# Kernel optimization log

Measured on AMD Instinct MI355X. Metric: run time of the kernel, lower is better.

## Reference

```python
import jax, jax.numpy as jnp
import numpy as np

BN_EPS = 1e-5


def conv1x1(x, w, b):
    # x: [B,C,H,W], w: [O,C], b: [O] -> [B,O,H,W]
    return jnp.einsum('bchw,oc->bohw', x, w) + b[None, :, None, None]


def setup_inputs() -> dict:
    key = jax.random.key(0)
    ks = jax.random.split(key, 11)
    B, C, H, W = 8, 1024, 64, 32
    hid = 64  # C * rd_ratio (1/16)
    s = 0.02
    return {
        'x': jax.random.normal(ks[0], (B, C, H, W), dtype=jnp.float32),
        'theta_w': jax.random.normal(ks[1], (hid, C), dtype=jnp.float32) * s,
        'theta_b': jax.random.normal(ks[2], (hid,), dtype=jnp.float32) * s,
        'phi_w': jax.random.normal(ks[3], (hid, C), dtype=jnp.float32) * s,
        'phi_b': jax.random.normal(ks[4], (hid,), dtype=jnp.float32) * s,
        'g_w': jax.random.normal(ks[5], (hid, C), dtype=jnp.float32) * s,
        'g_b': jax.random.normal(ks[6], (hid,), dtype=jnp.float32) * s,
        'w_w': jax.random.normal(ks[7], (C, hid), dtype=jnp.float32) * s,
        'w_b': jax.random.normal(ks[8], (C,), dtype=jnp.float32) * s,
        'bn_gamma': jax.random.normal(ks[9], (C,), dtype=jnp.float32) * 0.1 + 1.0,
        'bn_beta': jax.random.normal(ks[10], (C,), dtype=jnp.float32) * 0.1,
    }


def reference(x, theta_w, theta_b, phi_w, phi_b, g_w, g_b, w_w, w_b, bn_gamma, bn_beta):
    B, C, H, W = x.shape
    hid = theta_w.shape[0]
    N = H * W
    theta = conv1x1(x, theta_w, theta_b).reshape(B, hid, N).transpose(0, 2, 1)  # [B,N,d]
    phi = conv1x1(x, phi_w, phi_b).reshape(B, hid, N)                           # [B,d,N]
    g = conv1x1(x, g_w, g_b).reshape(B, hid, N).transpose(0, 2, 1)              # [B,N,d]
    f = jnp.einsum('bnd,bdm->bnm', theta, phi) / N                              # [B,N,N]
    y = jnp.einsum('bnm,bmd->bnd', f, g)                                        # [B,N,d]
    y = y.transpose(0, 2, 1).reshape(B, hid, H, W)
    wy = conv1x1(y, w_w, w_b)                                                   # [B,C,H,W]
    # BatchNorm2d in training mode: batch statistics over (B,H,W), biased variance
    mean = wy.mean(axis=(0, 2, 3), keepdims=True)
    var = wy.var(axis=(0, 2, 3), keepdims=True)
    norm = (wy - mean) * jax.lax.rsqrt(var + BN_EPS)
    out = norm * bn_gamma[None, :, None, None] + bn_beta[None, :, None, None]
    return out + x
```

## Files before the change

### kernel.cpp

```cpp
#include <hip/hip_runtime.h>

#define B_    8
#define C_    1024
#define HID   64
#define N_    2048
#define RTOT  192

typedef __attribute__((ext_vector_type(8))) short   bf16x8;
typedef __attribute__((ext_vector_type(8))) unsigned short ush8;
typedef __attribute__((ext_vector_type(4))) unsigned short ush4;
typedef __attribute__((ext_vector_type(4))) float   f32x4;

#define WSB_WBF   ((size_t)0)
#define WSB_TPG   ((size_t)393216)
#define WSB_THT   ((size_t)6684672)
#define WSB_M     ((size_t)8781824)
#define WSB_G     ((size_t)8912896)
#define WSB_S     ((size_t)9043968)
#define WSB_WMBF  ((size_t)9046016)
#define WSB_SC    ((size_t)10094592)
#define WSB_SH    ((size_t)10098688)

static __device__ __forceinline__ unsigned short f2bf(float f) {
    union { float f; unsigned u; } v; v.f = f;
    unsigned r = v.u + 0x7fffu + ((v.u >> 16) & 1u);
    return (unsigned short)(r >> 16);
}
static __device__ __forceinline__ float bf2f(unsigned short h) {
    union { unsigned u; float f; } v; v.u = ((unsigned)h) << 16;
    return v.f;
}

__global__ __launch_bounds__(256) void wcvt(
    const float* __restrict__ tw, const float* __restrict__ pw,
    const float* __restrict__ gw, unsigned short* __restrict__ wbf)
{
    int idx = blockIdx.x * 256 + threadIdx.x;
    int r = idx >> 10, k = idx & 1023;
    float v = (r < 64) ? tw[(size_t)r * 1024 + k]
            : (r < 128) ? pw[(size_t)(r - 64) * 1024 + k]
                        : gw[(size_t)(r - 128) * 1024 + k];
    wbf[idx] = f2bf(v);
}

__global__ __launch_bounds__(256, 2) void proj_mfma(
    const float* __restrict__ x, const unsigned short* __restrict__ wbf,
    const float* __restrict__ tb, const float* __restrict__ pb,
    const float* __restrict__ gb, unsigned short* __restrict__ tpgbf,
    unsigned short* __restrict__ thT)
{
    const int b = blockIdx.y, n0 = blockIdx.x * 32;
    const int t = threadIdx.x, w = t >> 6, L = t & 63;
    const int lr = L & 15, q = L >> 4;
    __shared__ unsigned short A_lds[32][520];

    const float* xb = x + (size_t)b * C_ * N_ + n0;
    const unsigned short* bp = wbf + ((size_t)(48 * w + lr)) * 1024 + q * 8;

    f32x4 acc[2][3] = {};

#pragma unroll
    for (int ph = 0; ph < 2; ph++) {
        if (ph) __syncthreads();
#pragma unroll
        for (int i = 0; i < 8; i++) {
            int p = t + 256 * i;
            int n4 = p & 7;
            int c  = ((p >> 3) << 1);
            f32x4 v0 = *(const f32x4*)(xb + (size_t)(512 * ph + c) * N_ + n4 * 4);
            f32x4 v1 = *(const f32x4*)(xb + (size_t)(512 * ph + c + 1) * N_ + n4 * 4);
#pragma unroll
            for (int r = 0; r < 4; r++) {
                unsigned val = (unsigned)f2bf(v0[r]) | ((unsigned)f2bf(v1[r]) << 16);
                *(unsigned*)&A_lds[n4 * 4 + r][c] = val;
            }
        }
        __syncthreads();
#pragma unroll
        for (int ks = 0; ks < 16; ks++) {
            const int kg = ph * 512 + ks * 32;
            bf16x8 B0 = *(const bf16x8*)(bp + kg);
            bf16x8 B1 = *(const bf16x8*)(bp + 16 * 1024 + kg);
            bf16x8 B2 = *(const bf16x8*)(bp + 32 * 1024 + kg);
            bf16x8 A0 = *(const bf16x8*)&A_lds[lr][ks * 32 + q * 8];
            bf16x8 A1 = *(const bf16x8*)&A_lds[16 + lr][ks * 32 + q * 8];
            acc[0][0] = __builtin_amdgcn_mfma_f32_16x16x32_bf16(A0, B0, acc[0][0], 0, 0, 0);
            acc[0][1] = __builtin_amdgcn_mfma_f32_16x16x32_bf16(A0, B1, acc[0][1], 0, 0, 0);
            acc[0][2] = __builtin_amdgcn_mfma_f32_16x16x32_bf16(A0, B2, acc[0][2], 0, 0, 0);
            acc[1][0] = __builtin_amdgcn_mfma_f32_16x16x32_bf16(A1, B0, acc[1][0], 0, 0, 0);
            acc[1][1] = __builtin_amdgcn_mfma_f32_16x16x32_bf16(A1, B1, acc[1][1], 0, 0, 0);
            acc[1][2] = __builtin_amdgcn_mfma_f32_16x16x32_bf16(A1, B2, acc[1][2], 0, 0, 0);
        }
    }

#pragma unroll
    for (int i = 0; i < 2; i++)
#pragma unroll
        for (int j = 0; j < 3; j++) {
            int rcol = 48 * w + 16 * j + lr;
            float bias = (rcol < 64) ? tb[rcol]
                       : (rcol < 128) ? pb[rcol - 64] : gb[rcol - 128];
            ush4 o;
#pragma unroll
            for (int rr = 0; rr < 4; rr++) o[rr] = f2bf(acc[i][j][rr] + bias);
            *(ush4*)(tpgbf + ((size_t)b * RTOT + rcol) * N_ + n0 + 16 * i + q * 4) = o;
            if (rcol < 64) {
#pragma unroll
                for (int rr = 0; rr < 4; rr++)
                    thT[((size_t)b * N_ + n0 + 16 * i + q * 4 + rr) * HID + rcol] = o[rr];
            }
        }
}

__global__ __launch_bounds__(256) void gram_mfma(
    const unsigned short* __restrict__ tpgbf, float* __restrict__ Mm,
    float* __restrict__ Gg, float* __restrict__ S)
{
    const int kc = blockIdx.x, p = blockIdx.y, b = blockIdx.z;
    const int t = threadIdx.x, w = t >> 6, L = t & 63;
    const int lr = L & 15, q = L >> 4;
    const unsigned short* base = tpgbf + (size_t)b * RTOT * N_;
    const unsigned short* Arow = base + (p ? 0 : (size_t)64 * N_);
    const unsigned short* Brow = base + (p ? 0 : (size_t)128 * N_);
    const unsigned short* ap = Arow + ((size_t)(16 * w + lr)) * N_ + kc * 256 + q * 8;
    const unsigned short* bp = Brow + ((size_t)lr) * N_ + kc * 256 + q * 8;

    bf16x8 ones;
#pragma unroll
    for (int j = 0; j < 8; j++) ones[j] = (short)0x3F80;

    f32x4 acc[4] = {};
    f32x4 accs = {};
#pragma unroll
    for (int it = 0; it < 8; ++it) {
        const int kn = it * 32;
        bf16x8 a = *(const bf16x8*)(ap + kn);
#pragma unroll
        for (int g = 0; g < 4; g++) {
            bf16x8 bb = *(const bf16x8*)(bp + (size_t)g * 16 * N_ + kn);
            acc[g] = __builtin_amdgcn_mfma_f32_16x16x32_bf16(a, bb, acc[g], 0, 0, 0);
        }
        if (p) accs = __builtin_amdgcn_mfma_f32_16x16x32_bf16(a, ones, accs, 0, 0, 0);
    }
    float* outp = (p ? Gg : Mm) + (size_t)b * HID * HID;
#pragma unroll
    for (int g = 0; g < 4; g++)
#pragma unroll
        for (int r = 0; r < 4; r++) {
            int row = 16 * w + q * 4 + r, col = 16 * g + lr;
            atomicAdd(outp + row * HID + col, acc[g][r]);
        }
    if (p && lr == 0) {
#pragma unroll
        for (int r = 0; r < 4; r++)
            atomicAdd(S + b * HID + 16 * w + q * 4 + r, accs[r]);
    }
}

__global__ __launch_bounds__(64) void wmstat(
    const float* __restrict__ ww, const float* __restrict__ Mm,
    const float* __restrict__ S, const float* __restrict__ G,
    const float* __restrict__ wb, const float* __restrict__ gamma,
    const float* __restrict__ beta, unsigned short* __restrict__ wmbf,
    float* __restrict__ scale, float* __restrict__ shift2)
{
    const int c = blockIdx.x, lane = threadIdx.x;
    const float wbc = wb[c];
    const float* wr = ww + (size_t)c * HID;
    float asum = 0.f, asq = 0.f;
    for (int b = 0; b < B_; b++) {
        const float* mr = Mm + ((size_t)b * HID + lane) * HID;
        float acc = 0.f;
#pragma unroll
        for (int d = 0; d < HID; d += 4) {
            float4 m4 = *(const float4*)(mr + d);
            acc += wr[d] * m4.x + wr[d + 1] * m4.y + wr[d + 2] * m4.z + wr[d + 3] * m4.w;
        }
        unsigned short us = f2bf(acc * (1.0f / N_));
        wmbf[((size_t)b * C_ + c) * HID + lane] = us;
        float v = bf2f(us);
        float sv = S[b * HID + lane];
        float t1 = v * sv;
        for (int off = 32; off; off >>= 1) t1 += __shfl_down(t1, off);
        t1 = __shfl(t1, 0);
        const float* Gb = G + (size_t)b * HID * HID + (size_t)lane * HID;
        float inner = 0.f;
        for (int f = 0; f < HID; f++) inner = fmaf(Gb[f], __shfl(v, f), inner);
        float qq = v * inner;
        for (int off = 32; off; off >>= 1) qq += __shfl_down(qq, off);
        qq = __shfl(qq, 0);
        asum += t1;
        asq  += qq + 2.f * wbc * t1;
    }
    const float cnt = (float)B_ * (float)N_;
    const float inv = 1.0f / cnt;
    float mean = (asum + cnt * wbc) * inv;
    float e2   = (asq + cnt * wbc * wbc) * inv;
    float var  = e2 - mean * mean;
    float sc   = gamma[c] * rsqrtf(var + 1e-5f);
    if (lane == 0) {
        scale[c]  = sc;
        shift2[c] = beta[c] - mean * sc + sc * wbc;
    }
}

__global__ __launch_bounds__(256) void finalk_mfma(
    const unsigned short* __restrict__ wmbf, const unsigned short* __restrict__ thT,
    const float* __restrict__ x, const float* __restrict__ scale,
    const float* __restrict__ shift2, float* __restrict__ out)
{
    const int b = blockIdx.z, c0 = blockIdx.y * 64, n0 = blockIdx.x * 64;
    const int t = threadIdx.x, w = t >> 6, L = t & 63;
    const int lr = L & 15, q = L >> 4;

    const unsigned short* ap = thT + ((size_t)b * N_ + n0 + 16 * w + lr) * HID + q * 8;
    const unsigned short* bp = wmbf + ((size_t)b * C_ + c0 + lr) * HID + q * 8;

    float4 xv[4];
    size_t xoff[4];
#pragma unroll
    for (int g = 0; g < 4; g++) {
        xoff[g] = ((size_t)b * C_ + c0 + 16 * g + lr) * N_ + n0 + 16 * w + q * 4;
        xv[g] = *(const float4*)(x + xoff[g]);
    }

    bf16x8 A0 = *(const bf16x8*)(ap);
    bf16x8 A1 = *(const bf16x8*)(ap + 32);
    f32x4 acc[4] = {};
#pragma unroll
    for (int g = 0; g < 4; g++) {
        bf16x8 Bg0 = *(const bf16x8*)(bp + (size_t)g * 16 * HID);
        bf16x8 Bg1 = *(const bf16x8*)(bp + (size_t)g * 16 * HID + 32);
        acc[g] = __builtin_amdgcn_mfma_f32_16x16x32_bf16(A0, Bg0, acc[g], 0, 0, 0);
        acc[g] = __builtin_amdgcn_mfma_f32_16x16x32_bf16(A1, Bg1, acc[g], 0, 0, 0);
    }
#pragma unroll
    for (int g = 0; g < 4; g++) {
        int c = c0 + 16 * g + lr;
        float sc = scale[c], sh = shift2[c];
        float4 o;
        o.x = fmaf(sc, acc[g][0], sh) + xv[g].x;
        o.y = fmaf(sc, acc[g][1], sh) + xv[g].y;
        o.z = fmaf(sc, acc[g][2], sh) + xv[g].z;
        o.w = fmaf(sc, acc[g][3], sh) + xv[g].w;
        *(float4*)(out + xoff[g]) = o;
    }
}

extern "C" void kernel_launch(void* const* d_in, const int* in_sizes, int n_in,
                              void* d_out, int out_size, void* d_ws, size_t ws_size,
                              hipStream_t stream)
{
    const float* x  = (const float*)d_in[0];
    const float* tw = (const float*)d_in[1];
    const float* tb = (const float*)d_in[2];
    const float* pw = (const float*)d_in[3];
    const float* pb = (const float*)d_in[4];
    const float* gw = (const float*)d_in[5];
    const float* gb = (const float*)d_in[6];
    const float* ww = (const float*)d_in[7];
    const float* wb = (const float*)d_in[8];
    const float* gamma = (const float*)d_in[9];
    const float* beta  = (const float*)d_in[10];
    float* out = (float*)d_out;

    char* ws = (char*)d_ws;
    unsigned short* wbf   = (unsigned short*)(ws + WSB_WBF);
    unsigned short* tpgbf = (unsigned short*)(ws + WSB_TPG);
    unsigned short* thT   = (unsigned short*)(ws + WSB_THT);
    float* Mm   = (float*)(ws + WSB_M);
    float* Gg   = (float*)(ws + WSB_G);
    float* S    = (float*)(ws + WSB_S);
    unsigned short* wmbf = (unsigned short*)(ws + WSB_WMBF);
    float* scl  = (float*)(ws + WSB_SC);
    float* shf  = (float*)(ws + WSB_SH);

    hipMemsetAsync(Mm, 0, (size_t)(2 * B_ * HID * HID + B_ * HID) * sizeof(float), stream);

    wcvt<<<dim3(RTOT * 1024 / 256), 256, 0, stream>>>(tw, pw, gw, wbf);
    proj_mfma<<<dim3(64, B_), 256, 0, stream>>>(x, wbf, tb, pb, gb, tpgbf, thT);
    gram_mfma<<<dim3(8, 2, B_), 256, 0, stream>>>(tpgbf, Mm, Gg, S);
    wmstat<<<C_, 64, 0, stream>>>(ww, Mm, S, Gg, wb, gamma, beta, wmbf, scl, shf);
    finalk_mfma<<<dim3(32, 16, B_), 256, 0, stream>>>(wmbf, thT, x, scl, shf, out);
}
```

Before: 219.8 us.

## Widen parallelism in projection, gram, and BN-stat kernels

The projection kernel moves to 512 threads, with each wave computing one 16-row half of the tile instead of both, which halves accumulators per wave. The gram kernel splits the N reduction into twice as many chunks, doubling the block count at the cost of more atomics. The BN-stat kernel handles all 8 batches in parallel across 8 waves and combines them through shared memory, replacing the serial batch loop. Together these aim to raise occupancy and shorten the latency-bound phases, at the cost of more atomic contention and duplicated B-fragment loads in the projection.

```diff
diff --git a/kernel.cpp b/kernel.cpp
--- a/kernel.cpp
+++ b/kernel.cpp
@@ -43,7 +43,7 @@
     wbf[idx] = f2bf(v);
 }
 
-__global__ __launch_bounds__(256, 2) void proj_mfma(
+__global__ __launch_bounds__(512, 4) void proj_mfma(
     const float* __restrict__ x, const unsigned short* __restrict__ wbf,
     const float* __restrict__ tb, const float* __restrict__ pb,
     const float* __restrict__ gb, unsigned short* __restrict__ tpgbf,
@@ -51,20 +51,21 @@
 {
     const int b = blockIdx.y, n0 = blockIdx.x * 32;
     const int t = threadIdx.x, w = t >> 6, L = t & 63;
+    const int og = w >> 1, nh = w & 1;
     const int lr = L & 15, q = L >> 4;
     __shared__ unsigned short A_lds[32][520];
 
     const float* xb = x + (size_t)b * C_ * N_ + n0;
-    const unsigned short* bp = wbf + ((size_t)(48 * w + lr)) * 1024 + q * 8;
-
-    f32x4 acc[2][3] = {};
+    const unsigned short* bp = wbf + ((size_t)(48 * og + lr)) * 1024 + q * 8;
+
+    f32x4 acc[3] = {};
 
 #pragma unroll
     for (int ph = 0; ph < 2; ph++) {
         if (ph) __syncthreads();
 #pragma unroll
-        for (int i = 0; i < 8; i++) {
-            int p = t + 256 * i;
+        for (int i = 0; i < 4; i++) {
+            int p = t + 512 * i;
             int n4 = p & 7;
             int c  = ((p >> 3) << 1);
             f32x4 v0 = *(const f32x4*)(xb + (size_t)(512 * ph + c) * N_ + n4 * 4);
@@ -82,34 +83,28 @@
             bf16x8 B0 = *(const bf16x8*)(bp + kg);
             bf16x8 B1 = *(const bf16x8*)(bp + 16 * 1024 + kg);
             bf16x8 B2 = *(const bf16x8*)(bp + 32 * 1024 + kg);
-            bf16x8 A0 = *(const bf16x8*)&A_lds[lr][ks * 32 + q * 8];
-            bf16x8 A1 = *(const bf16x8*)&A_lds[16 + lr][ks * 32 + q * 8];
-            acc[0][0] = __builtin_amdgcn_mfma_f32_16x16x32_bf16(A0, B0, acc[0][0], 0, 0, 0);
-            acc[0][1] = __builtin_amdgcn_mfma_f32_16x16x32_bf16(A0, B1, acc[0][1], 0, 0, 0);
-            acc[0][2] = __builtin_amdgcn_mfma_f32_16x16x32_bf16(A0, B2, acc[0][2], 0, 0, 0);
-            acc[1][0] = __builtin_amdgcn_mfma_f32_16x16x32_bf16(A1, B0, acc[1][0], 0, 0, 0);
-            acc[1][1] = __builtin_amdgcn_mfma_f32_16x16x32_bf16(A1, B1, acc[1][1], 0, 0, 0);
-            acc[1][2] = __builtin_amdgcn_mfma_f32_16x16x32_bf16(A1, B2, acc[1][2], 0, 0, 0);
-        }
-    }
-
-#pragma unroll
-    for (int i = 0; i < 2; i++)
-#pragma unroll
-        for (int j = 0; j < 3; j++) {
-            int rcol = 48 * w + 16 * j + lr;
-            float bias = (rcol < 64) ? tb[rcol]
-                       : (rcol < 128) ? pb[rcol - 64] : gb[rcol - 128];
-            ush4 o;
-#pragma unroll
-            for (int rr = 0; rr < 4; rr++) o[rr] = f2bf(acc[i][j][rr] + bias);
-            *(ush4*)(tpgbf + ((size_t)b * RTOT + rcol) * N_ + n0 + 16 * i + q * 4) = o;
-            if (rcol < 64) {
-#pragma unroll
-                for (int rr = 0; rr < 4; rr++)
-                    thT[((size_t)b * N_ + n0 + 16 * i + q * 4 + rr) * HID + rcol] = o[rr];
-            }
-        }
+            bf16x8 A0 = *(const bf16x8*)&A_lds[16 * nh + lr][ks * 32 + q * 8];
+            acc[0] = __builtin_amdgcn_mfma_f32_16x16x32_bf16(A0, B0, acc[0], 0, 0, 0);
+            acc[1] = __builtin_amdgcn_mfma_f32_16x16x32_bf16(A0, B1, acc[1], 0, 0, 0);
+            acc[2] = __builtin_amdgcn_mfma_f32_16x16x32_bf16(A0, B2, acc[2], 0, 0, 0);
+        }
+    }
+
+#pragma unroll
+    for (int j = 0; j < 3; j++) {
+        int rcol = 48 * og + 16 * j + lr;
+        float bias = (rcol < 64) ? tb[rcol]
+                   : (rcol < 128) ? pb[rcol - 64] : gb[rcol - 128];
+        ush4 o;
+#pragma unroll
+        for (int rr = 0; rr < 4; rr++) o[rr] = f2bf(acc[j][rr] + bias);
+        *(ush4*)(tpgbf + ((size_t)b * RTOT + rcol) * N_ + n0 + 16 * nh + q * 4) = o;
+        if (rcol < 64) {
+#pragma unroll
+            for (int rr = 0; rr < 4; rr++)
+                thT[((size_t)b * N_ + n0 + 16 * nh + q * 4 + rr) * HID + rcol] = o[rr];
+        }
+    }
 }
 
 __global__ __launch_bounds__(256) void gram_mfma(
@@ -122,8 +117,8 @@
     const unsigned short* base = tpgbf + (size_t)b * RTOT * N_;
     const unsigned short* Arow = base + (p ? 0 : (size_t)64 * N_);
     const unsigned short* Brow = base + (p ? 0 : (size_t)128 * N_);
-    const unsigned short* ap = Arow + ((size_t)(16 * w + lr)) * N_ + kc * 256 + q * 8;
-    const unsigned short* bp = Brow + ((size_t)lr) * N_ + kc * 256 + q * 8;
+    const unsigned short* ap = Arow + ((size_t)(16 * w + lr)) * N_ + kc * 128 + q * 8;
+    const unsigned short* bp = Brow + ((size_t)lr) * N_ + kc * 128 + q * 8;
 
     bf16x8 ones;
 #pragma unroll
@@ -132,7 +127,7 @@
     f32x4 acc[4] = {};
     f32x4 accs = {};
 #pragma unroll
-    for (int it = 0; it < 8; ++it) {
+    for (int it = 0; it < 4; ++it) {
         const int kn = it * 32;
         bf16x8 a = *(const bf16x8*)(ap + kn);
 #pragma unroll
@@ -157,48 +152,56 @@
     }
 }
 
-__global__ __launch_bounds__(64) void wmstat(
+__global__ __launch_bounds__(512) void wmstat(
     const float* __restrict__ ww, const float* __restrict__ Mm,
     const float* __restrict__ S, const float* __restrict__ G,
     const float* __restrict__ wb, const float* __restrict__ gamma,
     const float* __restrict__ beta, unsigned short* __restrict__ wmbf,
     float* __restrict__ scale, float* __restrict__ shift2)
 {
-    const int c = blockIdx.x, lane = threadIdx.x;
+    const int c = blockIdx.x;
+    const int t = threadIdx.x;
+    const int b = t >> 6, lane = t & 63;
     const float wbc = wb[c];
     const float* wr = ww + (size_t)c * HID;
-    float asum = 0.f, asq = 0.f;
-    for (int b = 0; b < B_; b++) {
-        const float* mr = Mm + ((size_t)b * HID + lane) * HID;
-        float acc = 0.f;
-#pragma unroll
-        for (int d = 0; d < HID; d += 4) {
-            float4 m4 = *(const float4*)(mr + d);
-            acc += wr[d] * m4.x + wr[d + 1] * m4.y + wr[d + 2] * m4.z + wr[d + 3] * m4.w;
-        }
-        unsigned short us = f2bf(acc * (1.0f / N_));
-        wmbf[((size_t)b * C_ + c) * HID + lane] = us;
-        float v = bf2f(us);
-        float sv = S[b * HID + lane];
-        float t1 = v * sv;
-        for (int off = 32; off; off >>= 1) t1 += __shfl_down(t1, off);
-        t1 = __shfl(t1, 0);
-        const float* Gb = G + (size_t)b * HID * HID + (size_t)lane * HID;
-        float inner = 0.f;
-        for (int f = 0; f < HID; f++) inner = fmaf(Gb[f], __shfl(v, f), inner);
-        float qq = v * inner;
-        for (int off = 32; off; off >>= 1) qq += __shfl_down(qq, off);
-        qq = __shfl(qq, 0);
-        asum += t1;
-        asq  += qq + 2.f * wbc * t1;
-    }
-    const float cnt = (float)B_ * (float)N_;
-    const float inv = 1.0f / cnt;
-    float mean = (asum + cnt * wbc) * inv;
-    float e2   = (asq + cnt * wbc * wbc) * inv;
-    float var  = e2 - mean * mean;
-    float sc   = gamma[c] * rsqrtf(var + 1e-5f);
+
+    const float* mr = Mm + ((size_t)b * HID + lane) * HID;
+    float acc = 0.f;
+#pragma unroll
+    for (int d = 0; d < HID; d += 4) {
+        float4 m4 = *(const float4*)(mr + d);
+        acc += wr[d] * m4.x + wr[d + 1] * m4.y + wr[d + 2] * m4.z + wr[d + 3] * m4.w;
+    }
+    unsigned short us = f2bf(acc * (1.0f / N_));
+    wmbf[((size_t)b * C_ + c) * HID + lane] = us;
+    float v = bf2f(us);
+    float sv = S[b * HID + lane];
+    float t1 = v * sv;
+    for (int off = 32; off; off >>= 1) t1 += __shfl_down(t1, off);
+    t1 = __shfl(t1, 0);
+    const float* Gb = G + (size_t)b * HID * HID + (size_t)lane * HID;
+    float inner = 0.f;
+    for (int f = 0; f < HID; f++) inner = fmaf(Gb[f], __shfl(v, f), inner);
+    float qq = v * inner;
+    for (int off = 32; off; off >>= 1) qq += __shfl_down(qq, off);
+    qq = __shfl(qq, 0);
+
+    __shared__ float red[16];
     if (lane == 0) {
+        red[b] = t1;
+        red[8 + b] = qq + 2.f * wbc * t1;
+    }
+    __syncthreads();
+    if (t == 0) {
+        float asum = 0.f, asq = 0.f;
+#pragma unroll
+        for (int i = 0; i < 8; i++) { asum += red[i]; asq += red[8 + i]; }
+        const float cnt = (float)B_ * (float)N_;
+        const float inv = 1.0f / cnt;
+        float mean = (asum + cnt * wbc) * inv;
+        float e2   = (asq + cnt * wbc * wbc) * inv;
+        float var  = e2 - mean * mean;
+        float sc   = gamma[c] * rsqrtf(var + 1e-5f);
         scale[c]  = sc;
         shift2[c] = beta[c] - mean * sc + sc * wbc;
     }
@@ -278,8 +281,8 @@
     hipMemsetAsync(Mm, 0, (size_t)(2 * B_ * HID * HID + B_ * HID) * sizeof(float), stream);
 
     wcvt<<<dim3(RTOT * 1024 / 256), 256, 0, stream>>>(tw, pw, gw, wbf);
-    proj_mfma<<<dim3(64, B_), 256, 0, stream>>>(x, wbf, tb, pb, gb, tpgbf, thT);
-    gram_mfma<<<dim3(8, 2, B_), 256, 0, stream>>>(tpgbf, Mm, Gg, S);
-    wmstat<<<C_, 64, 0, stream>>>(ww, Mm, S, Gg, wb, gamma, beta, wmbf, scl, shf);
+    proj_mfma<<<dim3(64, B_), 512, 0, stream>>>(x, wbf, tb, pb, gb, tpgbf, thT);
+    gram_mfma<<<dim3(16, 2, B_), 256, 0, stream>>>(tpgbf, Mm, Gg, S);
+    wmstat<<<C_, 512, 0, stream>>>(ww, Mm, S, Gg, wb, gamma, beta, wmbf, scl, shf);
     finalk_mfma<<<dim3(32, 16, B_), 256, 0, stream>>>(wmbf, thT, x, scl, shf, out);
 }
```

After: 235.8 us. +7.2%, slower.
